# Kernel tuning notes

Measured on AMD Instinct MI355X. Metric: run time of the kernel, lower is better.

The kernel has to match this reference:

```python
import jax, jax.numpy as jnp
import numpy as np

B, S, D, H = 2, 2048, 1024, 16
HD = D // H  # 64


def setup_inputs() -> dict:
    key = jax.random.key(0)
    ks = jax.random.split(key, 7)
    std = 1.0 / np.sqrt(D)
    return {
        "q": jax.random.normal(ks[0], (B, S, D), jnp.float32),
        "k": jax.random.normal(ks[1], (B, S, D), jnp.float32),
        "v": jax.random.normal(ks[2], (B, S, D), jnp.float32),
        "w_q": jax.random.normal(ks[3], (D, D), jnp.float32) * std,
        "w_k": jax.random.normal(ks[4], (D, D), jnp.float32) * std,
        "w_v": jax.random.normal(ks[5], (D, D), jnp.float32) * std,
        "w_o": jax.random.normal(ks[6], (D, D), jnp.float32) * std,
    }


def reference(q, k, v, w_q, w_k, w_v, w_o):
    # Linear (torch nn.Linear, no bias): y = x @ W.T
    Q = jnp.einsum('bsd,ed->bse', q, w_q)
    K = jnp.einsum('bsd,ed->bse', k, w_k)
    V = jnp.einsum('bsd,ed->bse', v, w_v)
    # split heads -> (B, H, S, HD)
    Qh = Q.reshape(B, S, H, HD).transpose(0, 2, 1, 3)
    Kh = K.reshape(B, S, H, HD).transpose(0, 2, 1, 3)
    Vh = V.reshape(B, S, H, HD).transpose(0, 2, 1, 3)
    scale = 1.0 / np.sqrt(HD).astype(np.float32)
    scores = jnp.einsum('bhqd,bhkd->bhqk', Qh, Kh) * scale  # [B,H,S,S]
    attn = jax.nn.softmax(scores, axis=-1)
    ctx = jnp.einsum('bhqk,bhkd->bhqd', attn, Vh)
    combined = ctx.transpose(0, 2, 1, 3).reshape(B, S, D)
    out = jnp.einsum('bsd,ed->bse', combined, w_o)
    return out, attn
```

## Files before the change

### kernel.cpp

```cpp
#include <hip/hip_runtime.h>
#include <hip/hip_bf16.h>
#include <cstdint>

#define B_ 2
#define S_ 2048
#define D_ 1024
#define H_ 16
#define HD_ 64

#define SCALE_LOG2 0.18033688011112042f

typedef __attribute__((ext_vector_type(8))) __bf16 bf16x8;
typedef __attribute__((ext_vector_type(8))) unsigned short ushort8;
typedef __attribute__((ext_vector_type(4))) unsigned short ushort4v;
typedef __attribute__((ext_vector_type(4))) float f32x4;

__device__ __forceinline__ unsigned short f2bf(float f) {
  __bf16 h = (__bf16)f;
  return __builtin_bit_cast(unsigned short, h);
}

__device__ __forceinline__ float bf2f(unsigned short u) {
  union { unsigned int i; float f; } v; v.i = ((unsigned int)u) << 16; return v.f;
}

__device__ __forceinline__ float fexp2(float x) {
#if __has_builtin(__builtin_amdgcn_exp2f)
  return __builtin_amdgcn_exp2f(x);
#else
  return exp2f(x);
#endif
}

__device__ __forceinline__ f32x4 mfma16(bf16x8 a, bf16x8 b, f32x4 c) {
  return __builtin_amdgcn_mfma_f32_16x16x32_bf16(a, b, c, 0, 0, 0);
}

#define LGKM_BARRIER()                                        \
  do {                                                        \
    asm volatile("s_waitcnt lgkmcnt(0)" ::: "memory");        \
    __builtin_amdgcn_s_barrier();                             \
  } while (0)

#define SWZ(r, sc) ((sc) ^ (((r) & 3) << 4))

__global__ __launch_bounds__(256) void proj_qkv_kernel(
    const float* __restrict__ qin, const float* __restrict__ kin,
    const float* __restrict__ vin, const float* __restrict__ wq,
    const float* __restrict__ wk, const float* __restrict__ wv,
    unsigned short* __restrict__ qh, unsigned short* __restrict__ kh,
    unsigned short* __restrict__ vt)
{
  __shared__ unsigned short As[128][40];
  __shared__ unsigned short Bs[128][40];

  const int z = blockIdx.z;
  const float* X = (z == 0) ? qin : (z == 1) ? kin : vin;
  const float* W = (z == 0) ? wq : (z == 1) ? wk : wv;
  unsigned short* dst = (z == 0) ? qh : (z == 1) ? kh : vt;
  const float osc = (z == 0) ? SCALE_LOG2 : 1.0f;

  const int lin = blockIdx.x + 8 * blockIdx.y;
  const int swz = (lin & 7) * 32 + (lin >> 3);
  const int bx = swz & 7, by = swz >> 3;

  const int tid = threadIdx.x;
  const int lane = tid & 63, wid = tid >> 6;
  const int c = lane & 15, g = lane >> 4;
  const int wr = wid >> 1, wc = wid & 1;
  const int m0 = by * 128, n0 = bx * 128;

  const int sr = tid >> 1, sh = tid & 1;
  const float* Ap = X + (size_t)(m0 + sr) * D_ + sh * 16;
  const float* Bp = W + (size_t)(n0 + sr) * D_ + sh * 16;

  float ar[16], br[16];
  f32x4 acc[4][4];
#pragma unroll
  for (int i = 0; i < 4; ++i)
#pragma unroll
    for (int j = 0; j < 4; ++j) acc[i][j] = (f32x4){0.f, 0.f, 0.f, 0.f};

  auto ldg_tile = [&](int kt) {
    const float* ap = Ap + kt * 32;
    const float* bp = Bp + kt * 32;
#pragma unroll
    for (int j = 0; j < 4; ++j) {
      *(f32x4*)(ar + 4 * j) = *(const f32x4*)(ap + 4 * j);
      *(f32x4*)(br + 4 * j) = *(const f32x4*)(bp + 4 * j);
    }
  };
  auto sts_tile = [&]() {
    unsigned short ta[16], tb[16];
#pragma unroll
    for (int j = 0; j < 16; ++j) { ta[j] = f2bf(ar[j]); tb[j] = f2bf(br[j]); }
    *(ushort8*)&As[sr][sh * 16]     = *(ushort8*)&ta[0];
    *(ushort8*)&As[sr][sh * 16 + 8] = *(ushort8*)&ta[8];
    *(ushort8*)&Bs[sr][sh * 16]     = *(ushort8*)&tb[0];
    *(ushort8*)&Bs[sr][sh * 16 + 8] = *(ushort8*)&tb[8];
  };

  ldg_tile(0);
  sts_tile();
  __syncthreads();

  for (int kt = 0; kt < 32; ++kt) {
    if (kt < 31) ldg_tile(kt + 1);
    bf16x8 af[4], bfr[4];
#pragma unroll
    for (int i = 0; i < 4; ++i) af[i]  = *(bf16x8*)&As[wr * 64 + i * 16 + c][g * 8];
#pragma unroll
    for (int i = 0; i < 4; ++i) bfr[i] = *(bf16x8*)&Bs[wc * 64 + i * 16 + c][g * 8];
#pragma unroll
    for (int mi = 0; mi < 4; ++mi)
#pragma unroll
      for (int ni = 0; ni < 4; ++ni)
        acc[mi][ni] = mfma16(af[mi], bfr[ni], acc[mi][ni]);
    __syncthreads();
    if (kt < 31) { sts_tile(); __syncthreads(); }
  }

#pragma unroll
  for (int mi = 0; mi < 4; ++mi) {
#pragma unroll
    for (int ni = 0; ni < 4; ++ni) {
      const int n = n0 + wc * 64 + ni * 16 + c;
      const int h = n >> 6, hd = n & 63;
      if (z < 2) {
#pragma unroll
        for (int r = 0; r < 4; ++r) {
          const int m = m0 + wr * 64 + mi * 16 + g * 4 + r;
          const int b = m >> 11, s = m & 2047;
          dst[((size_t)(b * H_ + h) * S_ + s) * HD_ + hd] = f2bf(acc[mi][ni][r] * osc);
        }
      } else {
        const int m = m0 + wr * 64 + mi * 16 + g * 4;
        const int b = m >> 11, s = m & 2047;
        ushort4v pk;
#pragma unroll
        for (int r = 0; r < 4; ++r) pk[r] = f2bf(acc[mi][ni][r]);
        *(ushort4v*)&dst[((size_t)(b * H_ + h) * HD_ + hd) * S_ + s] = pk;
      }
    }
  }
}

__global__ __launch_bounds__(256) void attn_kernel(
    const unsigned short* __restrict__ qh, const unsigned short* __restrict__ kh,
    const unsigned short* __restrict__ vt, float* __restrict__ attn,
    unsigned short* __restrict__ comb)
{
  __shared__ unsigned short Ks[64][64];
  __shared__ unsigned short Vs[64][64];
  __shared__ unsigned short Ps[4][16][88];

  const int tid = threadIdx.x;
  const int lane = tid & 63, w = tid >> 6;
  const int c = lane & 15, g = lane >> 4;

  const int lin = blockIdx.x;
  const int swz = (lin & 7) * 128 + (lin >> 3);
  const int bh = swz >> 5;
  const int q0 = (swz & 31) * 64;

  const unsigned short* Qb = qh + (size_t)bh * S_ * HD_;
  const unsigned short* Kb = kh + (size_t)bh * S_ * HD_;
  const unsigned short* Vb = vt + (size_t)bh * HD_ * S_;
  float* attnb = attn + (size_t)bh * S_ * S_;

  const int sr = tid >> 2;
  const int scol = (tid & 3) * 16;
  const int swcol = SWZ(sr, scol);

  bf16x8 aQ[2];
#pragma unroll
  for (int t = 0; t < 2; ++t)
    aQ[t] = *(const bf16x8*)(Qb + (size_t)(q0 + w * 16 + c) * HD_ + t * 32 + g * 8);

  const unsigned short* Kst = Kb + (size_t)sr * HD_ + scol;
  const unsigned short* Vst = Vb + (size_t)sr * S_ + scol;

  float l = 0.f;
  ushort8 kr0 = *(const ushort8*)Kst;
  ushort8 kr1 = *(const ushort8*)(Kst + 8);

  for (int kt = 0; kt < 32; ++kt) {
    *(ushort8*)&Ks[sr][swcol]     = kr0;
    *(ushort8*)&Ks[sr][swcol + 8] = kr1;
    LGKM_BARRIER();
    if (kt < 31) {
      const unsigned short* p = Kst + (size_t)(kt + 1) * 64 * HD_;
      kr0 = *(const ushort8*)p;
      kr1 = *(const ushort8*)(p + 8);
    }
#pragma unroll
    for (int ni = 0; ni < 4; ++ni) {
      f32x4 a = (f32x4){0.f, 0.f, 0.f, 0.f};
      a = mfma16(*(bf16x8*)&Ks[ni * 16 + c][SWZ(c, g * 8)],      aQ[0], a);
      a = mfma16(*(bf16x8*)&Ks[ni * 16 + c][SWZ(c, 32 + g * 8)], aQ[1], a);
      l += (fexp2(a[0]) + fexp2(a[1])) + (fexp2(a[2]) + fexp2(a[3]));
    }
    LGKM_BARRIER();
  }
  l += __shfl_xor(l, 16);
  l += __shfl_xor(l, 32);
  const float invl = 1.f / l;

  f32x4 ctx[4];
#pragma unroll
  for (int ni = 0; ni < 4; ++ni) ctx[ni] = (f32x4){0.f, 0.f, 0.f, 0.f};

  unsigned short* psrow = &Ps[w][c][g * 4];
  float* srow = attnb + (size_t)(q0 + w * 16 + g) * S_ + c * 4;

  kr0 = *(const ushort8*)Kst;
  kr1 = *(const ushort8*)(Kst + 8);
  ushort8 vr0 = *(const ushort8*)Vst;
  ushort8 vr1 = *(const ushort8*)(Vst + 8);

  for (int kt = 0; kt < 32; ++kt) {
    *(ushort8*)&Ks[sr][swcol]     = kr0;
    *(ushort8*)&Ks[sr][swcol + 8] = kr1;
    *(ushort8*)&Vs[sr][swcol]     = vr0;
    *(ushort8*)&Vs[sr][swcol + 8] = vr1;
    LGKM_BARRIER();
    if (kt < 31) {
      const unsigned short* p = Kst + (size_t)(kt + 1) * 64 * HD_;
      const unsigned short* q = Vst + (kt + 1) * 64;
      kr0 = *(const ushort8*)p;
      kr1 = *(const ushort8*)(p + 8);
      vr0 = *(const ushort8*)q;
      vr1 = *(const ushort8*)(q + 8);
    }

#pragma unroll
    for (int ni = 0; ni < 4; ++ni) {
      f32x4 a = (f32x4){0.f, 0.f, 0.f, 0.f};
      a = mfma16(*(bf16x8*)&Ks[ni * 16 + c][SWZ(c, g * 8)],      aQ[0], a);
      a = mfma16(*(bf16x8*)&Ks[ni * 16 + c][SWZ(c, 32 + g * 8)], aQ[1], a);
      ushort4v pk;
#pragma unroll
      for (int r = 0; r < 4; ++r) pk[r] = f2bf(fexp2(a[r]) * invl);
      *(ushort4v*)(psrow + ni * 16) = pk;
    }

    bf16x8 aP[2];
#pragma unroll
    for (int t = 0; t < 2; ++t) aP[t] = *(bf16x8*)&Ps[w][c][t * 32 + g * 8];
#pragma unroll
    for (int ni = 0; ni < 4; ++ni)
#pragma unroll
      for (int t = 0; t < 2; ++t)
        ctx[ni] = mfma16(aP[t],
                         *(bf16x8*)&Vs[ni * 16 + c][SWZ(c, t * 32 + g * 8)],
                         ctx[ni]);

#pragma unroll
    for (int it = 0; it < 4; ++it) {
      ushort4v pb = *(ushort4v*)&Ps[w][it * 4 + g][c * 4];
      f32x4 pf;
#pragma unroll
      for (int r = 0; r < 4; ++r) pf[r] = bf2f(pb[r]);
      __builtin_nontemporal_store(pf, (f32x4*)(srow + (size_t)it * 4 * S_ + kt * 64));
    }
    LGKM_BARRIER();
  }

  const int b = bh >> 4, h = bh & 15;
#pragma unroll
  for (int ni = 0; ni < 4; ++ni)
#pragma unroll
    for (int r = 0; r < 4; ++r)
      comb[(size_t)(b * S_ + q0 + w * 16 + g * 4 + r) * D_ + h * 64 + ni * 16 + c] =
          f2bf(ctx[ni][r]);
}

__global__ __launch_bounds__(256) void out_proj_kernel(
    const unsigned short* __restrict__ comb, const float* __restrict__ wo,
    float* __restrict__ out)
{
  __shared__ unsigned short As[128][40];
  __shared__ unsigned short Bs[128][40];

  const int lin = blockIdx.x + 8 * blockIdx.y;
  const int swz = (lin & 7) * 32 + (lin >> 3);
  const int bx = swz & 7, by = swz >> 3;

  const int tid = threadIdx.x;
  const int lane = tid & 63, wid = tid >> 6;
  const int c = lane & 15, g = lane >> 4;
  const int wr = wid >> 1, wc = wid & 1;
  const int m0 = by * 128, n0 = bx * 128;
  const int sr = tid >> 1, sh = tid & 1;

  const unsigned short* Apb = comb + (size_t)(m0 + sr) * D_ + sh * 16;
  const float* Bpb = wo + (size_t)(n0 + sr) * D_ + sh * 16;

  ushort8 ar2[2];
  float br[16];
  f32x4 acc[4][4];
#pragma unroll
  for (int i = 0; i < 4; ++i)
#pragma unroll
    for (int j = 0; j < 4; ++j) acc[i][j] = (f32x4){0.f, 0.f, 0.f, 0.f};

  auto ldg_tile = [&](int kt) {
    ar2[0] = *(const ushort8*)(Apb + kt * 32);
    ar2[1] = *(const ushort8*)(Apb + kt * 32 + 8);
#pragma unroll
    for (int j = 0; j < 4; ++j)
      *(f32x4*)(br + 4 * j) = *(const f32x4*)(Bpb + kt * 32 + 4 * j);
  };
  auto sts_tile = [&]() {
    *(ushort8*)&As[sr][sh * 16]     = ar2[0];
    *(ushort8*)&As[sr][sh * 16 + 8] = ar2[1];
    unsigned short tb[16];
#pragma unroll
    for (int j = 0; j < 16; ++j) tb[j] = f2bf(br[j]);
    *(ushort8*)&Bs[sr][sh * 16]     = *(ushort8*)&tb[0];
    *(ushort8*)&Bs[sr][sh * 16 + 8] = *(ushort8*)&tb[8];
  };

  ldg_tile(0);
  sts_tile();
  __syncthreads();

  for (int kt = 0; kt < 32; ++kt) {
    if (kt < 31) ldg_tile(kt + 1);
    bf16x8 af[4], bfr[4];
#pragma unroll
    for (int i = 0; i < 4; ++i) af[i]  = *(bf16x8*)&As[wr * 64 + i * 16 + c][g * 8];
#pragma unroll
    for (int i = 0; i < 4; ++i) bfr[i] = *(bf16x8*)&Bs[wc * 64 + i * 16 + c][g * 8];
#pragma unroll
    for (int mi = 0; mi < 4; ++mi)
#pragma unroll
      for (int ni = 0; ni < 4; ++ni)
        acc[mi][ni] = mfma16(af[mi], bfr[ni], acc[mi][ni]);
    __syncthreads();
    if (kt < 31) { sts_tile(); __syncthreads(); }
  }

#pragma unroll
  for (int mi = 0; mi < 4; ++mi)
#pragma unroll
    for (int ni = 0; ni < 4; ++ni)
#pragma unroll
      for (int r = 0; r < 4; ++r) {
        const int m = m0 + wr * 64 + mi * 16 + g * 4 + r;
        const int n = n0 + wc * 64 + ni * 16 + c;
        out[(size_t)m * D_ + n] = acc[mi][ni][r];
      }
}

extern "C" void kernel_launch(void* const* d_in, const int* in_sizes, int n_in,
                              void* d_out, int out_size, void* d_ws, size_t ws_size,
                              hipStream_t stream)
{
  const float* q  = (const float*)d_in[0];
  const float* k  = (const float*)d_in[1];
  const float* v  = (const float*)d_in[2];
  const float* wq = (const float*)d_in[3];
  const float* wk = (const float*)d_in[4];
  const float* wv = (const float*)d_in[5];
  const float* wo = (const float*)d_in[6];

  float* out  = (float*)d_out;
  float* attn = out + (size_t)B_ * S_ * D_;

  const size_t NE = (size_t)B_ * S_ * D_;
  unsigned short* qh   = (unsigned short*)d_ws;
  unsigned short* kh   = qh + NE;
  unsigned short* vt   = kh + NE;
  unsigned short* comb = vt + NE;

  proj_qkv_kernel<<<dim3(8, 32, 3), dim3(256), 0, stream>>>(q, k, v, wq, wk, wv, qh, kh, vt);
  attn_kernel<<<dim3(1024), dim3(256), 0, stream>>>(qh, kh, vt, attn, comb);
  out_proj_kernel<<<dim3(8, 32), dim3(256), 0, stream>>>(comb, wo, out);
}
```

Before: 232.6 us.

## Process two 64-row query tiles per block, fusing B's row-sum pass into A's

Each attention block now handles 128 query rows as two 64-row halves, launching 512 blocks instead of 1024. The row-sum pass for the second half is folded into the main pass of the first half, so the block makes three K sweeps instead of four for two tiles. This cuts redundant K/V loads and QK^T recomputation per query row. In exchange it holds more registers, which may lower occupancy, and the grid is halved, which can reduce parallelism and latency hiding.

```diff
diff --git a/kernel.cpp b/kernel.cpp
--- a/kernel.cpp
+++ b/kernel.cpp
@@ -159,9 +159,9 @@
   const int c = lane & 15, g = lane >> 4;
 
   const int lin = blockIdx.x;
-  const int swz = (lin & 7) * 128 + (lin >> 3);
-  const int bh = swz >> 5;
-  const int q0 = (swz & 31) * 64;
+  const int swz = (lin & 7) * 64 + (lin >> 3);
+  const int bh = swz >> 4;
+  const int q0 = (swz & 15) * 128;
 
   const unsigned short* Qb = qh + (size_t)bh * S_ * HD_;
   const unsigned short* Kb = kh + (size_t)bh * S_ * HD_;
@@ -172,107 +172,187 @@
   const int scol = (tid & 3) * 16;
   const int swcol = SWZ(sr, scol);
 
-  bf16x8 aQ[2];
-#pragma unroll
-  for (int t = 0; t < 2; ++t)
-    aQ[t] = *(const bf16x8*)(Qb + (size_t)(q0 + w * 16 + c) * HD_ + t * 32 + g * 8);
+  bf16x8 aQA[2], aQB[2];
+#pragma unroll
+  for (int t = 0; t < 2; ++t) {
+    aQA[t] = *(const bf16x8*)(Qb + (size_t)(q0 + w * 16 + c) * HD_ + t * 32 + g * 8);
+    aQB[t] = *(const bf16x8*)(Qb + (size_t)(q0 + 64 + w * 16 + c) * HD_ + t * 32 + g * 8);
+  }
 
   const unsigned short* Kst = Kb + (size_t)sr * HD_ + scol;
   const unsigned short* Vst = Vb + (size_t)sr * S_ + scol;
 
-  float l = 0.f;
-  ushort8 kr0 = *(const ushort8*)Kst;
-  ushort8 kr1 = *(const ushort8*)(Kst + 8);
-
-  for (int kt = 0; kt < 32; ++kt) {
-    *(ushort8*)&Ks[sr][swcol]     = kr0;
-    *(ushort8*)&Ks[sr][swcol + 8] = kr1;
-    LGKM_BARRIER();
-    if (kt < 31) {
-      const unsigned short* p = Kst + (size_t)(kt + 1) * 64 * HD_;
-      kr0 = *(const ushort8*)p;
-      kr1 = *(const ushort8*)(p + 8);
-    }
-#pragma unroll
-    for (int ni = 0; ni < 4; ++ni) {
-      f32x4 a = (f32x4){0.f, 0.f, 0.f, 0.f};
-      a = mfma16(*(bf16x8*)&Ks[ni * 16 + c][SWZ(c, g * 8)],      aQ[0], a);
-      a = mfma16(*(bf16x8*)&Ks[ni * 16 + c][SWZ(c, 32 + g * 8)], aQ[1], a);
-      l += (fexp2(a[0]) + fexp2(a[1])) + (fexp2(a[2]) + fexp2(a[3]));
-    }
-    LGKM_BARRIER();
-  }
-  l += __shfl_xor(l, 16);
-  l += __shfl_xor(l, 32);
-  const float invl = 1.f / l;
-
-  f32x4 ctx[4];
-#pragma unroll
-  for (int ni = 0; ni < 4; ++ni) ctx[ni] = (f32x4){0.f, 0.f, 0.f, 0.f};
+  float lA = 0.f, lB = 0.f;
+  {
+    ushort8 kr0 = *(const ushort8*)Kst;
+    ushort8 kr1 = *(const ushort8*)(Kst + 8);
+    for (int kt = 0; kt < 32; ++kt) {
+      *(ushort8*)&Ks[sr][swcol]     = kr0;
+      *(ushort8*)&Ks[sr][swcol + 8] = kr1;
+      LGKM_BARRIER();
+      if (kt < 31) {
+        const unsigned short* p = Kst + (size_t)(kt + 1) * 64 * HD_;
+        kr0 = *(const ushort8*)p;
+        kr1 = *(const ushort8*)(p + 8);
+      }
+#pragma unroll
+      for (int ni = 0; ni < 4; ++ni) {
+        bf16x8 k0 = *(bf16x8*)&Ks[ni * 16 + c][SWZ(c, g * 8)];
+        bf16x8 k1 = *(bf16x8*)&Ks[ni * 16 + c][SWZ(c, 32 + g * 8)];
+        f32x4 a = (f32x4){0.f, 0.f, 0.f, 0.f};
+        a = mfma16(k0, aQA[0], a);
+        a = mfma16(k1, aQA[1], a);
+        lA += (fexp2(a[0]) + fexp2(a[1])) + (fexp2(a[2]) + fexp2(a[3]));
+      }
+      LGKM_BARRIER();
+    }
+  }
+  lA += __shfl_xor(lA, 16);
+  lA += __shfl_xor(lA, 32);
+  const float invlA = 1.f / lA;
+
+  f32x4 ctxA[4], ctxB[4];
+#pragma unroll
+  for (int ni = 0; ni < 4; ++ni) {
+    ctxA[ni] = (f32x4){0.f, 0.f, 0.f, 0.f};
+    ctxB[ni] = (f32x4){0.f, 0.f, 0.f, 0.f};
+  }
 
   unsigned short* psrow = &Ps[w][c][g * 4];
-  float* srow = attnb + (size_t)(q0 + w * 16 + g) * S_ + c * 4;
-
-  kr0 = *(const ushort8*)Kst;
-  kr1 = *(const ushort8*)(Kst + 8);
-  ushort8 vr0 = *(const ushort8*)Vst;
-  ushort8 vr1 = *(const ushort8*)(Vst + 8);
-
-  for (int kt = 0; kt < 32; ++kt) {
-    *(ushort8*)&Ks[sr][swcol]     = kr0;
-    *(ushort8*)&Ks[sr][swcol + 8] = kr1;
-    *(ushort8*)&Vs[sr][swcol]     = vr0;
-    *(ushort8*)&Vs[sr][swcol + 8] = vr1;
-    LGKM_BARRIER();
-    if (kt < 31) {
-      const unsigned short* p = Kst + (size_t)(kt + 1) * 64 * HD_;
-      const unsigned short* q = Vst + (kt + 1) * 64;
-      kr0 = *(const ushort8*)p;
-      kr1 = *(const ushort8*)(p + 8);
-      vr0 = *(const ushort8*)q;
-      vr1 = *(const ushort8*)(q + 8);
-    }
-
-#pragma unroll
-    for (int ni = 0; ni < 4; ++ni) {
-      f32x4 a = (f32x4){0.f, 0.f, 0.f, 0.f};
-      a = mfma16(*(bf16x8*)&Ks[ni * 16 + c][SWZ(c, g * 8)],      aQ[0], a);
-      a = mfma16(*(bf16x8*)&Ks[ni * 16 + c][SWZ(c, 32 + g * 8)], aQ[1], a);
-      ushort4v pk;
-#pragma unroll
-      for (int r = 0; r < 4; ++r) pk[r] = f2bf(fexp2(a[r]) * invl);
-      *(ushort4v*)(psrow + ni * 16) = pk;
-    }
-
-    bf16x8 aP[2];
-#pragma unroll
-    for (int t = 0; t < 2; ++t) aP[t] = *(bf16x8*)&Ps[w][c][t * 32 + g * 8];
-#pragma unroll
-    for (int ni = 0; ni < 4; ++ni)
-#pragma unroll
-      for (int t = 0; t < 2; ++t)
-        ctx[ni] = mfma16(aP[t],
-                         *(bf16x8*)&Vs[ni * 16 + c][SWZ(c, t * 32 + g * 8)],
-                         ctx[ni]);
-
-#pragma unroll
-    for (int it = 0; it < 4; ++it) {
-      ushort4v pb = *(ushort4v*)&Ps[w][it * 4 + g][c * 4];
-      f32x4 pf;
-#pragma unroll
-      for (int r = 0; r < 4; ++r) pf[r] = bf2f(pb[r]);
-      __builtin_nontemporal_store(pf, (f32x4*)(srow + (size_t)it * 4 * S_ + kt * 64));
-    }
-    LGKM_BARRIER();
+  float* srowA = attnb + (size_t)(q0 + w * 16 + g) * S_ + c * 4;
+  float* srowB = attnb + (size_t)(q0 + 64 + w * 16 + g) * S_ + c * 4;
+
+  {
+    ushort8 kr0 = *(const ushort8*)Kst;
+    ushort8 kr1 = *(const ushort8*)(Kst + 8);
+    ushort8 vr0 = *(const ushort8*)Vst;
+    ushort8 vr1 = *(const ushort8*)(Vst + 8);
+
+    for (int kt = 0; kt < 32; ++kt) {
+      *(ushort8*)&Ks[sr][swcol]     = kr0;
+      *(ushort8*)&Ks[sr][swcol + 8] = kr1;
+      *(ushort8*)&Vs[sr][swcol]     = vr0;
+      *(ushort8*)&Vs[sr][swcol + 8] = vr1;
+      LGKM_BARRIER();
+      if (kt < 31) {
+        const unsigned short* p = Kst + (size_t)(kt + 1) * 64 * HD_;
+        const unsigned short* q = Vst + (kt + 1) * 64;
+        kr0 = *(const ushort8*)p;
+        kr1 = *(const ushort8*)(p + 8);
+        vr0 = *(const ushort8*)q;
+        vr1 = *(const ushort8*)(q + 8);
+      }
+
+#pragma unroll
+      for (int ni = 0; ni < 4; ++ni) {
+        bf16x8 k0 = *(bf16x8*)&Ks[ni * 16 + c][SWZ(c, g * 8)];
+        bf16x8 k1 = *(bf16x8*)&Ks[ni * 16 + c][SWZ(c, 32 + g * 8)];
+        f32x4 a = (f32x4){0.f, 0.f, 0.f, 0.f};
+        a = mfma16(k0, aQA[0], a);
+        a = mfma16(k1, aQA[1], a);
+        ushort4v pk;
+#pragma unroll
+        for (int r = 0; r < 4; ++r) pk[r] = f2bf(fexp2(a[r]) * invlA);
+        *(ushort4v*)(psrow + ni * 16) = pk;
+        f32x4 b = (f32x4){0.f, 0.f, 0.f, 0.f};
+        b = mfma16(k0, aQB[0], b);
+        b = mfma16(k1, aQB[1], b);
+        lB += (fexp2(b[0]) + fexp2(b[1])) + (fexp2(b[2]) + fexp2(b[3]));
+      }
+
+      bf16x8 aP[2];
+#pragma unroll
+      for (int t = 0; t < 2; ++t) aP[t] = *(bf16x8*)&Ps[w][c][t * 32 + g * 8];
+#pragma unroll
+      for (int ni = 0; ni < 4; ++ni)
+#pragma unroll
+        for (int t = 0; t < 2; ++t)
+          ctxA[ni] = mfma16(aP[t],
+                            *(bf16x8*)&Vs[ni * 16 + c][SWZ(c, t * 32 + g * 8)],
+                            ctxA[ni]);
+
+#pragma unroll
+      for (int it = 0; it < 4; ++it) {
+        ushort4v pb = *(ushort4v*)&Ps[w][it * 4 + g][c * 4];
+        f32x4 pf;
+#pragma unroll
+        for (int r = 0; r < 4; ++r) pf[r] = bf2f(pb[r]);
+        __builtin_nontemporal_store(pf, (f32x4*)(srowA + (size_t)it * 4 * S_ + kt * 64));
+      }
+      LGKM_BARRIER();
+    }
+  }
+  lB += __shfl_xor(lB, 16);
+  lB += __shfl_xor(lB, 32);
+  const float invlB = 1.f / lB;
+
+  {
+    ushort8 kr0 = *(const ushort8*)Kst;
+    ushort8 kr1 = *(const ushort8*)(Kst + 8);
+    ushort8 vr0 = *(const ushort8*)Vst;
+    ushort8 vr1 = *(const ushort8*)(Vst + 8);
+
+    for (int kt = 0; kt < 32; ++kt) {
+      *(ushort8*)&Ks[sr][swcol]     = kr0;
+      *(ushort8*)&Ks[sr][swcol + 8] = kr1;
+      *(ushort8*)&Vs[sr][swcol]     = vr0;
+      *(ushort8*)&Vs[sr][swcol + 8] = vr1;
+      LGKM_BARRIER();
+      if (kt < 31) {
+        const unsigned short* p = Kst + (size_t)(kt + 1) * 64 * HD_;
+        const unsigned short* q = Vst + (kt + 1) * 64;
+        kr0 = *(const ushort8*)p;
+        kr1 = *(const ushort8*)(p + 8);
+        vr0 = *(const ushort8*)q;
+        vr1 = *(const ushort8*)(q + 8);
+      }
+
+#pragma unroll
+      for (int ni = 0; ni < 4; ++ni) {
+        bf16x8 k0 = *(bf16x8*)&Ks[ni * 16 + c][SWZ(c, g * 8)];
+        bf16x8 k1 = *(bf16x8*)&Ks[ni * 16 + c][SWZ(c, 32 + g * 8)];
+        f32x4 b = (f32x4){0.f, 0.f, 0.f, 0.f};
+        b = mfma16(k0, aQB[0], b);
+        b = mfma16(k1, aQB[1], b);
+        ushort4v pk;
+#pragma unroll
+        for (int r = 0; r < 4; ++r) pk[r] = f2bf(fexp2(b[r]) * invlB);
+        *(ushort4v*)(psrow + ni * 16) = pk;
+      }
+
+      bf16x8 aP[2];
+#pragma unroll
+      for (int t = 0; t < 2; ++t) aP[t] = *(bf16x8*)&Ps[w][c][t * 32 + g * 8];
+#pragma unroll
+      for (int ni = 0; ni < 4; ++ni)
+#pragma unroll
+        for (int t = 0; t < 2; ++t)
+          ctxB[ni] = mfma16(aP[t],
+                            *(bf16x8*)&Vs[ni * 16 + c][SWZ(c, t * 32 + g * 8)],
+                            ctxB[ni]);
+
+#pragma unroll
+      for (int it = 0; it < 4; ++it) {
+        ushort4v pb = *(ushort4v*)&Ps[w][it * 4 + g][c * 4];
+        f32x4 pf;
+#pragma unroll
+        for (int r = 0; r < 4; ++r) pf[r] = bf2f(pb[r]);
+        __builtin_nontemporal_store(pf, (f32x4*)(srowB + (size_t)it * 4 * S_ + kt * 64));
+      }
+      LGKM_BARRIER();
+    }
   }
 
   const int b = bh >> 4, h = bh & 15;
 #pragma unroll
   for (int ni = 0; ni < 4; ++ni)
 #pragma unroll
-    for (int r = 0; r < 4; ++r)
+    for (int r = 0; r < 4; ++r) {
       comb[(size_t)(b * S_ + q0 + w * 16 + g * 4 + r) * D_ + h * 64 + ni * 16 + c] =
-          f2bf(ctx[ni][r]);
+          f2bf(ctxA[ni][r]);
+      comb[(size_t)(b * S_ + q0 + 64 + w * 16 + g * 4 + r) * D_ + h * 64 + ni * 16 + c] =
+          f2bf(ctxB[ni][r]);
+    }
 }
 
 __global__ __launch_bounds__(256) void out_proj_kernel(
@@ -375,6 +455,6 @@
   unsigned short* comb = vt + NE;
 
   proj_qkv_kernel<<<dim3(8, 32, 3), dim3(256), 0, stream>>>(q, k, v, wq, wk, wv, qh, kh, vt);
-  attn_kernel<<<dim3(1024), dim3(256), 0, stream>>>(qh, kh, vt, attn, comb);
+  attn_kernel<<<dim3(512), dim3(256), 0, stream>>>(qh, kh, vt, attn, comb);
   out_proj_kernel<<<dim3(8, 32), dim3(256), 0, stream>>>(comb, wo, out);
 }
```

Result: faster. 227.0 us (-2.4%).
